# Performance work log

Hardware: AMD Instinct MI355X
Metric: run time of the kernel (lower is better)

The kernel has to match this reference:

```python
import jax, jax.numpy as jnp
import numpy as np

N, E, B = 50000, 800000, 1000
NODE_DIN, BB_DOUT, DHID, K = 32, 64, 64, 3
GLOB_DIN, EMBED_DIN = 64, 64
CIN = BB_DOUT + NODE_DIN  # 96


def setup_inputs() -> dict:
    key = jax.random.key(0)
    ks = jax.random.split(key, 24)

    def w(k, shape, fan_in):
        return jax.random.normal(k, shape, jnp.float32) / np.float32(np.sqrt(fan_in))

    inp = dict(
        x=jax.random.normal(ks[0], (N, NODE_DIN), jnp.float32),
        u=jax.random.normal(ks[1], (B, GLOB_DIN), jnp.float32),
        z=jax.random.normal(ks[2], (N, BB_DOUT), jnp.float32),
        edge_index=jax.random.randint(ks[3], (2, E), 0, N),
        edge_weight=jax.random.uniform(ks[4], (E,), jnp.float32),
        batch=jnp.sort(jax.random.randint(ks[5], (N,), 0, B)),
        batch_size=B,
        prev_h=jax.random.normal(ks[6], (N, DHID), jnp.float32),
    )
    # six ChebConvs of GConvGRU: x-convs take CIN, h-convs take DHID; all output DHID
    for i, nm in enumerate(["xz", "hz", "xr", "hr", "xh", "hh"]):
        cin = CIN if nm[0] == "x" else DHID
        inp[f"W{nm}"] = w(ks[7 + 2 * i], (K, cin, DHID), cin * K)
        inp[f"b{nm}"] = jnp.zeros((DHID,), jnp.float32)
    inp["Wg"] = w(ks[20], (GLOB_DIN, EMBED_DIN), GLOB_DIN)
    inp["bg"] = jnp.zeros((EMBED_DIN,), jnp.float32)
    return inp


def _cheb(xin, W, b, src, dst, w_norm, n):
    """ChebConv with sym norm, lambda_max=2 -> L_hat = -D^-1/2 A D^-1/2 (diag cancels)."""
    def prop(t):  # L_hat @ t  ([N,C])
        return -jax.ops.segment_sum(w_norm[:, None] * t[src], dst, num_segments=n)

    out = xin @ W[0] + b
    tx_prev = xin
    tx = None
    if W.shape[0] > 1:
        tx = prop(xin)
        out = out + tx @ W[1]
    for k in range(2, W.shape[0]):
        tx_new = 2.0 * prop(tx) - tx_prev
        out = out + tx_new @ W[k]
        tx_prev, tx = tx, tx_new
    return out


def reference(x, u, z, edge_index, edge_weight, batch, batch_size, prev_h,
              Wxz, bxz, Whz, bhz, Wxr, bxr, Whr, bhr, Wxh, bxh, Whh, bhh, Wg, bg):
    n = x.shape[0]
    src, dst = edge_index[0], edge_index[1]
    deg = jax.ops.segment_sum(edge_weight, src, num_segments=n)
    deg_safe = jnp.where(deg > 0, deg, 1.0)
    dinv = jnp.where(deg > 0, jax.lax.rsqrt(deg_safe), 0.0)
    w_norm = dinv[src] * edge_weight * dinv[dst]

    xin = jnp.concatenate([z, x], axis=-1)  # [N, CIN]
    Z = jax.nn.sigmoid(_cheb(xin, Wxz, bxz, src, dst, w_norm, n)
                       + _cheb(prev_h, Whz, bhz, src, dst, w_norm, n))
    R = jax.nn.sigmoid(_cheb(xin, Wxr, bxr, src, dst, w_norm, n)
                       + _cheb(prev_h, Whr, bhr, src, dst, w_norm, n))
    Ht = jnp.tanh(_cheb(xin, Wxh, bxh, src, dst, w_norm, n)
                  + _cheb(prev_h * R, Whh, bhh, src, dst, w_norm, n))
    h = Z * prev_h + (1.0 - Z) * Ht

    graph_emb = jax.ops.segment_sum(z, batch, num_segments=batch_size)  # [B, BB_DOUT]
    global_emb = jax.nn.relu(u @ Wg + bg)                                # [B, EMBED_DIN]
    fused = jnp.concatenate([graph_emb, global_emb], axis=-1)           # [B, 128]
    return fused, h
```

## Files before the change

kernel.cpp:

```cpp
#include <hip/hip_runtime.h>

#define NN 50000
#define EE 800000
#define BB 1000
#define NB 196
#define NR 5
#define RS 10496
#define NC 32
#define CHUNK 25000

#define BUILDBLKS 15625
#define PACKBLKS 204
#define FINBLKS 782

typedef unsigned short u16;
typedef __attribute__((ext_vector_type(8))) short bf16x8;
typedef __attribute__((ext_vector_type(4))) float f32x4;

static __device__ __forceinline__ u16 f2b(float f) {
    union { float f; unsigned u; } v;
    v.f = f;
    unsigned r = v.u + 0x7fffu + ((v.u >> 16) & 1u);
    return (u16)(r >> 16);
}

static __device__ __forceinline__ float b2f(short s) {
    union { unsigned u; float f; } c;
    c.u = ((unsigned)(u16)s) << 16;
    return c.f;
}

__global__ __launch_bounds__(512) void k_hist(
    const int* __restrict__ src, const int* __restrict__ dst,
    const float* __restrict__ ew, float* __restrict__ deg_p,
    int* __restrict__ cnt_p, int* __restrict__ rank, int* __restrict__ ctr) {
    __shared__ float sdeg[RS];
    __shared__ unsigned scnt2[RS / 2];
    if (blockIdx.x == 0 && threadIdx.x == 0) atomicExch(ctr, 0);
    int r = blockIdx.x % NR;
    int c = blockIdx.x / NR;
    int base = r * RS;
    for (int i = threadIdx.x; i < RS; i += 512) sdeg[i] = 0.f;
    for (int i = threadIdx.x; i < RS / 2; i += 512) scnt2[i] = 0u;
    __syncthreads();
    int e0 = c * CHUNK;
    for (int j = threadIdx.x; j < CHUNK; j += 512) {
        int e = e0 + j;
        int s = src[e], d = dst[e];
        int sl = s - base, dl = d - base;
        if ((unsigned)sl < RS) atomicAdd(&sdeg[sl], ew[e]);
        if ((unsigned)dl < RS) {
            unsigned old = atomicAdd(&scnt2[dl >> 1], (dl & 1) ? 65536u : 1u);
            rank[e] = (int)((old >> ((dl & 1) * 16)) & 0xffffu);
        }
    }
    __syncthreads();
    int lim = (NN - base < RS) ? (NN - base) : RS;
    for (int i = threadIdx.x; i < lim; i += 512) {
        deg_p[(size_t)c * NN + base + i] = sdeg[i];
        cnt_p[(size_t)c * NN + base + i] = (int)((scnt2[i >> 1] >> ((i & 1) * 16)) & 0xffffu);
    }
}

__global__ __launch_bounds__(512) void k_build(
    const float* __restrict__ z, const float* __restrict__ x,
    const float* __restrict__ ph, u16* __restrict__ A0,
    const float* __restrict__ Wxz, const float* __restrict__ Wxr,
    const float* __restrict__ Wxh, const float* __restrict__ Whz,
    const float* __restrict__ Whr, const float* __restrict__ Whh,
    u16* __restrict__ Wp, u16* __restrict__ W3p) {
    int bid = blockIdx.x;
    if (bid < BUILDBLKS) {
        int i = bid * 512 + threadIdx.x;
        int n = i / 160, c = i - n * 160;
        float v;
        if (c < 64) v = z[n * 64 + c];
        else if (c < 96) v = x[n * 32 + (c - 64)];
        else v = ph[n * 64 + (c - 96)];
        A0[(size_t)n * 160 + c] = f2b(v);
        return;
    }
    int idx = (bid - BUILDBLKS) * 512 + threadIdx.x;
    if (idx < 15 * 12 * 512) {
        int j = idx & 7, l = (idx >> 3) & 63;
        int ct = (idx >> 9) % 12, s = (idx >> 9) / 12;
        int k = 32 * s + (l >> 4) * 8 + j;
        int g = ct >> 2;
        int c = 16 * (ct & 3) + (l & 15);
        int lvl = k / 160, kk = k - lvl * 160;
        float val;
        if (kk < 96) {
            const float* W = (g == 0) ? Wxz : ((g == 1) ? Wxr : Wxh);
            if (lvl == 0)      val = W[kk * 64 + c] - W[(192 + kk) * 64 + c];
            else if (lvl == 1) val = W[(96 + kk) * 64 + c];
            else               val = 2.f * W[(192 + kk) * 64 + c];
        } else if (g == 2) {
            val = 0.f;
        } else {
            const float* W = (g == 0) ? Whz : Whr;
            int kh = kk - 96;
            if (lvl == 0)      val = W[kh * 64 + c] - W[(128 + kh) * 64 + c];
            else if (lvl == 1) val = W[(64 + kh) * 64 + c];
            else               val = 2.f * W[(128 + kh) * 64 + c];
        }
        Wp[idx] = f2b(val);
    } else {
        int i2 = idx - 15 * 12 * 512;
        int j = i2 & 7, l = (i2 >> 3) & 63;
        int ct = (i2 >> 9) & 3, s = i2 >> 11;
        int k = 32 * s + (l >> 4) * 8 + j;
        int ki = k >> 6, kr = k & 63;
        int c = 16 * ct + (l & 15);
        float val;
        if (ki == 0)      val = Whh[kr * 64 + c] - Whh[(128 + kr) * 64 + c];
        else if (ki == 1) val = Whh[(64 + kr) * 64 + c];
        else              val = 2.f * Whh[(128 + kr) * 64 + c];
        W3p[i2] = f2b(val);
    }
}

__global__ __launch_bounds__(256) void k_scan(
    const int* __restrict__ cnt_p, const float* __restrict__ deg_p,
    int* __restrict__ cnt, int* __restrict__ cbase, float* __restrict__ dinv,
    int* __restrict__ bsum, int* __restrict__ ctr) {
    __shared__ int s[256];
    int b = blockIdx.x;
    int i = b * 256 + threadIdx.x;
    int v = 0;
    float d = 0.f;
    if (i < NN) {
#pragma unroll
        for (int p = 0; p < NC; p++) {
            v += cnt_p[(size_t)p * NN + i];
            d += deg_p[(size_t)p * NN + i];
        }
        cnt[i] = v;
        dinv[i] = d > 0.f ? rsqrtf(d) : 0.f;
    }
    s[threadIdx.x] = v;
    __syncthreads();
    for (int off = 1; off < 256; off <<= 1) {
        int t = (threadIdx.x >= off) ? s[threadIdx.x - off] : 0;
        __syncthreads();
        s[threadIdx.x] += t;
        __syncthreads();
    }
    int incl = s[threadIdx.x];
    if (threadIdx.x == 255) atomicExch(&bsum[b], s[255]);
    __threadfence();
    if (threadIdx.x == 0) {
        atomicAdd(ctr, 1);
        while (atomicAdd(ctr, 0) < NB) __builtin_amdgcn_s_sleep(8);
    }
    __syncthreads();
    __threadfence();
    int pv = (threadIdx.x < b) ? atomicAdd(&bsum[threadIdx.x], 0) : 0;
    s[threadIdx.x] = pv;
    __syncthreads();
    for (int off = 128; off > 0; off >>= 1) {
        if (threadIdx.x < off) s[threadIdx.x] += s[threadIdx.x + off];
        __syncthreads();
    }
    int prefix = s[0];
    if (i < NN) {
        int run = prefix + incl - v;
#pragma unroll
        for (int c = 0; c < NC; c++) {
            cbase[(size_t)c * NN + i] = run;
            run += cnt_p[(size_t)c * NN + i];
        }
    }
}

__global__ void k_scatter(const int* __restrict__ src, const int* __restrict__ dst,
                          const float* __restrict__ ew, const float* __restrict__ dinv,
                          const int* __restrict__ cbase, const int* __restrict__ rank,
                          uint2* __restrict__ csr8) {
    int e = blockIdx.x * 256 + threadIdx.x;
    if (e >= EE) return;
    int c = e / CHUNK;
    int d = dst[e], s = src[e];
    int pos = cbase[(size_t)c * NN + d] + rank[e];
    float w = dinv[s] * ew[e] * dinv[d];
    csr8[pos] = make_uint2((unsigned)s, __float_as_uint(w));
}

template <int C, int BS, int INS, int OUTS>
__global__ __launch_bounds__(BS) void k_pull(
    const u16* __restrict__ in, u16* __restrict__ out,
    const uint2* __restrict__ csr8, const int* __restrict__ row_ptr,
    const int* __restrict__ cnt) {
    constexpr int TPR = C / 16;
    int tid = blockIdx.x * BS + threadIdx.x;
    int r = tid / TPR;
    int c16 = (tid - r * TPR) * 16;
    if (r >= NN) return;
    int s0 = row_ptr[r], n = cnt[r];
    float acc[16];
#pragma unroll
    for (int k = 0; k < 16; k++) acc[k] = 0.f;
    const u16* inp = in + c16;
    uint2 e = (n > 0) ? csr8[s0] : make_uint2(0u, 0u);
    for (int j = 0; j < n; j++) {
        uint2 ec = e;
        if (j + 1 < n) e = csr8[s0 + j + 1];
        float w = __uint_as_float(ec.y);
        const u16* p = inp + (size_t)ec.x * INS;
        bf16x8 v0 = *(const bf16x8*)(p);
        bf16x8 v1 = *(const bf16x8*)(p + 8);
#pragma unroll
        for (int k = 0; k < 8; k++) {
            acc[k] += w * b2f(v0[k]);
            acc[8 + k] += w * b2f(v1[k]);
        }
    }
    bf16x8 p0, p1;
#pragma unroll
    for (int k = 0; k < 8; k++) {
        p0[k] = (short)f2b(-acc[k]);
        p1[k] = (short)f2b(-acc[8 + k]);
    }
    u16* op = out + (size_t)r * OUTS + c16;
    *(bf16x8*)(op) = p0;
    *(bf16x8*)(op + 8) = p1;
}

__global__ __launch_bounds__(256) void k_gates_mfma(
    const u16* __restrict__ A0, const u16* __restrict__ A1, const u16* __restrict__ A2,
    const u16* __restrict__ Wp,
    const float* __restrict__ bxz, const float* __restrict__ bhz,
    const float* __restrict__ bxr, const float* __restrict__ bhr,
    const float* __restrict__ bxh,
    u16* __restrict__ Zb16, u16* __restrict__ Hx16, u16* __restrict__ A3) {
    int wv = (blockIdx.x * 256 + threadIdx.x) >> 6;
    int lane = threadIdx.x & 63;
    int r0 = wv * 16;
    if (r0 >= NN) return;
    int q = lane >> 4, j0 = lane & 15;

    f32x4 acc[12];
#pragma unroll
    for (int i = 0; i < 12; i++) acc[i] = (f32x4){0.f, 0.f, 0.f, 0.f};

    size_t rofs = (size_t)(r0 + j0) * 160 + q * 8;
    const u16* arow[3] = {A0 + rofs, A1 + rofs, A2 + rofs};
#pragma unroll
    for (int s = 0; s < 15; s++) {
        bf16x8 a = *(const bf16x8*)(arow[s / 5] + 32 * (s % 5));
        const u16* bp = Wp + (size_t)(s * 12) * 512 + lane * 8;
#pragma unroll
        for (int ct = 0; ct < 12; ct++) {
            bf16x8 b = *(const bf16x8*)(bp + ct * 512);
            acc[ct] = __builtin_amdgcn_mfma_f32_16x16x32_bf16(a, b, acc[ct], 0, 0, 0);
        }
    }

#pragma unroll
    for (int ct = 0; ct < 4; ct++) {
        int j = 16 * ct + j0;
        float bz = bxz[j] + bhz[j];
        float br = bxr[j] + bhr[j];
        float bh = bxh[j];
#pragma unroll
        for (int reg = 0; reg < 4; reg++) {
            int r = r0 + q * 4 + reg;
            size_t i = (size_t)r * 64 + j;
            float zp = acc[ct][reg] + bz;
            float rp = acc[ct + 4][reg] + br;
            float hp = acc[ct + 8][reg] + bh;
            float zv = 1.f / (1.f + expf(-zp));
            float rv = 1.f / (1.f + expf(-rp));
            float phv = b2f((short)A0[(size_t)r * 160 + 96 + j]);
            Zb16[i] = f2b(zv);
            Hx16[i] = f2b(hp);
            A3[(size_t)r * 192 + j] = f2b(rv * phv);
        }
    }
}

__global__ __launch_bounds__(256) void k_final_tail(
    const u16* __restrict__ A3, const u16* __restrict__ W3p,
    const float* __restrict__ bhh, const u16* __restrict__ Hx16,
    const u16* __restrict__ Zb16, const u16* __restrict__ A0,
    float* __restrict__ outh,
    const float* __restrict__ z, const int* __restrict__ batch,
    const float* __restrict__ u, const float* __restrict__ Wg,
    const float* __restrict__ bg, float* __restrict__ outF) {
    if (blockIdx.x >= FINBLKS) {
        int b = ((blockIdx.x - FINBLKS) * 256 + threadIdx.x) >> 6;
        int lane = threadIdx.x & 63;
        if (b >= BB) return;
        int lo = 0, hi = NN;
        while (lo < hi) {
            int m = (lo + hi) >> 1;
            if (batch[m] < b) lo = m + 1; else hi = m;
        }
        int start = lo;
        hi = NN;
        while (lo < hi) {
            int m = (lo + hi) >> 1;
            if (batch[m] < b + 1) lo = m + 1; else hi = m;
        }
        int end = lo;
        float acc = 0.f;
        for (int n = start; n < end; n++) acc += z[(size_t)n * 64 + lane];
        float g = bg[lane];
        const float* ur = u + (size_t)b * 64;
        for (int k = 0; k < 64; k++) g += ur[k] * Wg[k * 64 + lane];
        g = fmaxf(g, 0.f);
        outF[(size_t)b * 128 + lane] = acc;
        outF[(size_t)b * 128 + 64 + lane] = g;
        return;
    }
    int wv = (blockIdx.x * 256 + threadIdx.x) >> 6;
    int lane = threadIdx.x & 63;
    int r0 = wv * 16;
    if (r0 >= NN) return;
    int q = lane >> 4, j0 = lane & 15;

    f32x4 acc[4];
#pragma unroll
    for (int i = 0; i < 4; i++) acc[i] = (f32x4){0.f, 0.f, 0.f, 0.f};

    const u16* arow = A3 + (size_t)(r0 + j0) * 192 + q * 8;
#pragma unroll
    for (int s = 0; s < 6; s++) {
        bf16x8 a = *(const bf16x8*)(arow + 32 * s);
        const u16* bp = W3p + (size_t)(s * 4) * 512 + lane * 8;
#pragma unroll
        for (int ct = 0; ct < 4; ct++) {
            bf16x8 b = *(const bf16x8*)(bp + ct * 512);
            acc[ct] = __builtin_amdgcn_mfma_f32_16x16x32_bf16(a, b, acc[ct], 0, 0, 0);
        }
    }

#pragma unroll
    for (int ct = 0; ct < 4; ct++) {
        int j = 16 * ct + j0;
        float bh = bhh[j];
#pragma unroll
        for (int reg = 0; reg < 4; reg++) {
            int r = r0 + q * 4 + reg;
            size_t i = (size_t)r * 64 + j;
            float ht = tanhf(b2f((short)Hx16[i]) + acc[ct][reg] + bh);
            float zv = b2f((short)Zb16[i]);
            float phv = b2f((short)A0[(size_t)r * 160 + 96 + j]);
            outh[i] = zv * phv + (1.f - zv) * ht;
        }
    }
}

extern "C" void kernel_launch(void* const* d_in, const int* in_sizes, int n_in,
                              void* d_out, int out_size, void* d_ws, size_t ws_size,
                              hipStream_t stream) {
    const float* x  = (const float*)d_in[0];
    const float* u  = (const float*)d_in[1];
    const float* z  = (const float*)d_in[2];
    const int*   ei = (const int*)d_in[3];
    const float* ew = (const float*)d_in[4];
    const int* batch = (const int*)d_in[5];
    const float* ph = (const float*)d_in[7];
    const float *Wxz = (const float*)d_in[8],  *bxz = (const float*)d_in[9];
    const float *Whz = (const float*)d_in[10], *bhz = (const float*)d_in[11];
    const float *Wxr = (const float*)d_in[12], *bxr = (const float*)d_in[13];
    const float *Whr = (const float*)d_in[14], *bhr = (const float*)d_in[15];
    const float *Wxh = (const float*)d_in[16], *bxh = (const float*)d_in[17];
    const float *Whh = (const float*)d_in[18], *bhh = (const float*)d_in[19];
    const float *Wg  = (const float*)d_in[20], *bg  = (const float*)d_in[21];
    const int* src = ei;
    const int* dst = ei + EE;

    char* wsb = (char*)d_ws;
    size_t o = 0;
    auto alloc = [&](size_t bytes) {
        void* p = wsb + o;
        o += (bytes + 255) & ~(size_t)255;
        return p;
    };
    float* deg_p = (float*)alloc((size_t)NC * NN * 4);
    int*   cnt_p = (int*)alloc((size_t)NC * NN * 4);
    int*   cnt   = (int*)alloc(NN * 4);
    int*   cbase = (int*)alloc((size_t)NC * NN * 4);
    int*   rank  = (int*)alloc((size_t)EE * 4);
    float* dinv  = (float*)alloc(NN * 4);
    int*   bsum  = (int*)alloc(256 * 4);
    int*   ctr   = (int*)alloc(256);
    uint2* csr8  = (uint2*)alloc((size_t)EE * 8);
    u16*   Zb16  = (u16*)alloc((size_t)NN * 64 * 2);
    u16*   Hx16  = (u16*)alloc((size_t)NN * 64 * 2);
    u16*   A0    = (u16*)alloc((size_t)NN * 160 * 2);
    u16*   A1    = (u16*)alloc((size_t)NN * 160 * 2);
    u16*   A2    = (u16*)alloc((size_t)NN * 160 * 2);
    u16*   A3    = (u16*)alloc((size_t)NN * 192 * 2);
    u16*   Wp    = (u16*)alloc(15 * 12 * 512 * 2);
    u16*   W3p   = (u16*)alloc(6 * 4 * 512 * 2);

    float* outF = (float*)d_out;
    float* outH = outF + (size_t)BB * 128;

    const int BLK = 256;
    const int gE = (EE + BLK - 1) / BLK;
    const int gPull160 = (NN + 31) / 32;
    const int gPull64 = (NN + 63) / 64;
    const int gTail = (BB * 64 + BLK - 1) / BLK;
    int* row_ptr = cbase;

    k_hist<<<NR * NC, 512, 0, stream>>>(src, dst, ew, deg_p, cnt_p, rank, ctr);

    k_build<<<BUILDBLKS + PACKBLKS, 512, 0, stream>>>(
        z, x, ph, A0, Wxz, Wxr, Wxh, Whz, Whr, Whh, Wp, W3p);

    k_scan<<<NB, 256, 0, stream>>>(cnt_p, deg_p, cnt, cbase, dinv, bsum, ctr);

    k_scatter<<<gE, BLK, 0, stream>>>(src, dst, ew, dinv, cbase, rank, csr8);

    k_pull<160, 320, 160, 160><<<gPull160, 320, 0, stream>>>(A0, A1, csr8, row_ptr, cnt);
    k_pull<160, 320, 160, 160><<<gPull160, 320, 0, stream>>>(A1, A2, csr8, row_ptr, cnt);

    k_gates_mfma<<<FINBLKS, BLK, 0, stream>>>(A0, A1, A2, Wp, bxz, bhz, bxr, bhr, bxh,
                                              Zb16, Hx16, A3);

    k_pull<64, 256, 192, 192><<<gPull64, 256, 0, stream>>>(A3, A3 + 64, csr8, row_ptr, cnt);
    k_pull<64, 256, 192, 192><<<gPull64, 256, 0, stream>>>(A3 + 64, A3 + 128, csr8, row_ptr, cnt);

    k_final_tail<<<FINBLKS + gTail, BLK, 0, stream>>>(A3, W3p, bhh, Hx16, Zb16, A0, outH,
                                                      z, batch, u, Wg, bg, outF);
}
```

Baseline: 431.1 us.

## Fuse scan and edge scatter via grid barrier; split histogram into more ranges

Merges the scan kernel and the edge-scatter kernel into one launch of NB blocks. A software grid barrier built on an atomic counter with sleep-polling lets every block finish writing cbase and dinv before the grid-strided scatter begins. It also doubles the number of node ranges in the histogram and halves the range size, giving the histogram kernel more blocks. This removes one launch and its gap, at the cost of running the scatter on only 196 blocks. The barrier relies on all 196 blocks being resident at once and on the ctr counter's expected value matching how many times it has already been incremented.

```diff
diff --git a/kernel.cpp b/kernel.cpp
--- a/kernel.cpp
+++ b/kernel.cpp
@@ -4,8 +4,8 @@
 #define EE 800000
 #define BB 1000
 #define NB 196
-#define NR 5
-#define RS 10496
+#define NR 10
+#define RS 5248
 #define NC 32
 #define CHUNK 25000
 
@@ -119,10 +119,13 @@
     }
 }
 
-__global__ __launch_bounds__(256) void k_scan(
+__global__ __launch_bounds__(256) void k_scan_scatter(
     const int* __restrict__ cnt_p, const float* __restrict__ deg_p,
     int* __restrict__ cnt, int* __restrict__ cbase, float* __restrict__ dinv,
-    int* __restrict__ bsum, int* __restrict__ ctr) {
+    int* __restrict__ bsum, int* __restrict__ ctr,
+    const int* __restrict__ src, const int* __restrict__ dst,
+    const float* __restrict__ ew, const int* __restrict__ rank,
+    uint2* __restrict__ csr8) {
     __shared__ int s[256];
     int b = blockIdx.x;
     int i = b * 256 + threadIdx.x;
@@ -170,19 +173,20 @@
             run += cnt_p[(size_t)c * NN + i];
         }
     }
-}
-
-__global__ void k_scatter(const int* __restrict__ src, const int* __restrict__ dst,
-                          const float* __restrict__ ew, const float* __restrict__ dinv,
-                          const int* __restrict__ cbase, const int* __restrict__ rank,
-                          uint2* __restrict__ csr8) {
-    int e = blockIdx.x * 256 + threadIdx.x;
-    if (e >= EE) return;
-    int c = e / CHUNK;
-    int d = dst[e], s = src[e];
-    int pos = cbase[(size_t)c * NN + d] + rank[e];
-    float w = dinv[s] * ew[e] * dinv[d];
-    csr8[pos] = make_uint2((unsigned)s, __float_as_uint(w));
+    __threadfence();
+    if (threadIdx.x == 0) {
+        atomicAdd(ctr, 1);
+        while (atomicAdd(ctr, 0) < 2 * NB) __builtin_amdgcn_s_sleep(8);
+    }
+    __syncthreads();
+    __threadfence();
+    for (int e = b * 256 + threadIdx.x; e < EE; e += NB * 256) {
+        int c = e / CHUNK;
+        int dd = dst[e], ss = src[e];
+        int pos = cbase[(size_t)c * NN + dd] + rank[e];
+        float w = dinv[ss] * ew[e] * dinv[dd];
+        csr8[pos] = make_uint2((unsigned)ss, __float_as_uint(w));
+    }
 }
 
 template <int C, int BS, int INS, int OUTS>
@@ -399,7 +403,6 @@
     float* outH = outF + (size_t)BB * 128;
 
     const int BLK = 256;
-    const int gE = (EE + BLK - 1) / BLK;
     const int gPull160 = (NN + 31) / 32;
     const int gPull64 = (NN + 63) / 64;
     const int gTail = (BB * 64 + BLK - 1) / BLK;
@@ -410,9 +413,8 @@
     k_build<<<BUILDBLKS + PACKBLKS, 512, 0, stream>>>(
         z, x, ph, A0, Wxz, Wxr, Wxh, Whz, Whr, Whh, Wp, W3p);
 
-    k_scan<<<NB, 256, 0, stream>>>(cnt_p, deg_p, cnt, cbase, dinv, bsum, ctr);
-
-    k_scatter<<<gE, BLK, 0, stream>>>(src, dst, ew, dinv, cbase, rank, csr8);
+    k_scan_scatter<<<NB, 256, 0, stream>>>(cnt_p, deg_p, cnt, cbase, dinv, bsum, ctr,
+                                           src, dst, ew, rank, csr8);
 
     k_pull<160, 320, 160, 160><<<gPull160, 320, 0, stream>>>(A0, A1, csr8, row_ptr, cnt);
     k_pull<160, 320, 160, 160><<<gPull160, 320, 0, stream>>>(A1, A2, csr8, row_ptr, cnt);
```

New measurement: 469.2 us. +8.8%, slower.
